# Optimization experiments

Hardware: AMD Instinct MI355X
Metric: run time of the kernel (lower is better)

The kernel has to match this reference:

```python
import jax, jax.numpy as jnp
import numpy as np

LOC_SIZE, LOC_EMB = 100000, 256
TIM_SIZE, TIM_EMB = 48, 64
UID_SIZE, UID_EMB = 5000, 128
HID = 512
B, T = 64, 128
L_HIST, G = 1024, 4  # 256 history groups of size 4


def setup_inputs() -> dict:
    key = jax.random.key(0)
    ks = jax.random.split(key, 16)
    s = 0.02
    inp = {
        "loc": jax.random.randint(ks[0], (B, T), 0, LOC_SIZE),
        "tim": jax.random.randint(ks[1], (B, T), 0, TIM_SIZE),
        "input_lengths": jax.random.randint(ks[2], (B,), 1, T + 1),
        "history_loc": jax.random.randint(ks[3], (B, L_HIST), 0, LOC_SIZE),
        "history_tim": jax.random.randint(ks[4], (B, L_HIST), 0, TIM_SIZE),
        "history_uid": jax.random.randint(ks[5], (B, L_HIST), 0, UID_SIZE),
        "group_size": G,
        "emb_loc": jax.random.normal(ks[6], (LOC_SIZE, LOC_EMB), jnp.float32) * s,
        "emb_tim": jax.random.normal(ks[7], (TIM_SIZE, TIM_EMB), jnp.float32) * s,
        "emb_uid": jax.random.normal(ks[8], (UID_SIZE, UID_EMB), jnp.float32) * s,
        "W_attn": jax.random.normal(ks[9], (HID, LOC_EMB + TIM_EMB + UID_EMB), jnp.float32) * s,
        "b_attn": jnp.zeros((HID,), jnp.float32),
        "W_ih": jax.random.normal(ks[10], (3 * HID, LOC_EMB + TIM_EMB), jnp.float32) * s,
        "b_ih": jnp.zeros((3 * HID,), jnp.float32),
        "W_hh": jax.random.normal(ks[11], (3 * HID, HID), jnp.float32) * s,
        "b_hh": jnp.zeros((3 * HID,), jnp.float32),
        "W_final": jax.random.normal(ks[12], (UID_SIZE, 3 * HID), jnp.float32) * s,
        "b_final": jnp.zeros((UID_SIZE,), jnp.float32),
    }
    return inp


def _gru(x_seq, W_ih, b_ih, W_hh, b_hh):
    # x_seq: [T, B, Din] -> outputs [T, B, H], PyTorch gate order (r, z, n)
    H = W_hh.shape[1]
    gx = jnp.einsum("tbd,gd->tbg", x_seq, W_ih) + b_ih  # [T,B,3H]
    h0 = jnp.zeros((x_seq.shape[1], H), x_seq.dtype)

    def step(h, gx_t):
        gh = h @ W_hh.T + b_hh
        xr, xz, xn = jnp.split(gx_t, 3, axis=-1)
        hr, hz, hn = jnp.split(gh, 3, axis=-1)
        r = jax.nn.sigmoid(xr + hr)
        z = jax.nn.sigmoid(xz + hz)
        n = jnp.tanh(xn + r * hn)
        h_new = (1.0 - z) * n + z * h
        return h_new, h_new

    _, outs = jax.lax.scan(step, h0, gx)
    return outs  # [T,B,H]


def reference(loc, tim, input_lengths, history_loc, history_tim, history_uid,
              group_size, emb_loc, emb_tim, emb_uid, W_attn, b_attn,
              W_ih, b_ih, W_hh, b_hh, W_final, b_final):
    Bn, Tn = loc.shape
    # current-trajectory embeddings -> GRU (dropout is identity in eval)
    x = jnp.concatenate([emb_loc[loc], emb_tim[tim]], axis=-1)  # [B,T,Din]
    outs = _gru(jnp.swapaxes(x, 0, 1), W_ih, b_ih, W_hh, b_hh)  # [T,B,H]
    outs = jnp.swapaxes(outs, 0, 1)                              # [B,T,H]
    last = outs[jnp.arange(Bn), input_lengths - 1]               # [B,H]

    # history pooling: groups of size G; uid emb averaged within group,
    # loc/tim embeddings taken at each group's first element
    Gc = group_size
    n_groups = history_uid.shape[1] // Gc
    uid_h = emb_uid[history_uid].reshape(Bn, n_groups, Gc, -1).mean(axis=2)  # [B,N,Du]
    loc_h = emb_loc[history_loc[:, ::Gc]]                                    # [B,N,Dl]
    tim_h = emb_tim[history_tim[:, ::Gc]]                                    # [B,N,Dt]
    hist = jnp.concatenate([loc_h, tim_h, uid_h], axis=-1)
    hist = jnp.tanh(jnp.einsum("bnd,hd->bnh", hist, W_attn) + b_attn)        # [B,N,H]

    # 'dot' attention: replaces the nested python-loop scoring
    energies = jnp.einsum("bh,bnh->bn", last, hist)
    attn_w = jax.nn.softmax(energies, axis=-1)
    context = jnp.einsum("bn,bnh->bh", attn_w, hist)

    out = jnp.concatenate([last, context, last], axis=-1)  # [B,3H]
    y = out @ W_final.T + b_final                          # [B,U]
    # original assigns y (one row) into score[t] of shape [T,U] -> broadcast over T
    score = jnp.broadcast_to(y[:, None, :], (Bn, Tn, y.shape[-1]))
    return score
```

## Files before the change

kernel.cpp:

```cpp
#include <hip/hip_runtime.h>
#include <hip/hip_bf16.h>


typedef __attribute__((ext_vector_type(8))) short bf16x8;
typedef __attribute__((ext_vector_type(4))) float f32x4;
typedef __attribute__((ext_vector_type(4))) unsigned short u16x4;
typedef __attribute__((ext_vector_type(2))) unsigned long long u64x2;
typedef unsigned long long u64;

__device__ inline unsigned short f2bf(float x) {
  __hip_bfloat16 b = __float2bfloat16(x);
  return __builtin_bit_cast(unsigned short, b);
}
__device__ inline bf16x8 pack8(float4 a, float4 b) {
  bf16x8 w;
  w[0]=(short)f2bf(a.x); w[1]=(short)f2bf(a.y); w[2]=(short)f2bf(a.z); w[3]=(short)f2bf(a.w);
  w[4]=(short)f2bf(b.x); w[5]=(short)f2bf(b.y); w[6]=(short)f2bf(b.z); w[7]=(short)f2bf(b.w);
  return w;
}

__global__ __launch_bounds__(256)
void gemm_gx_f(const int* __restrict__ loc, const int* __restrict__ tim,
               const float* __restrict__ eloc, const float* __restrict__ etim,
               const float* __restrict__ W_ih, const float* __restrict__ b_ih,
               float* __restrict__ gx) {
  constexpr int LDR = 40, K = 320, N = 1536;
  __shared__ short Asl[128 * LDR];
  __shared__ short Bsl[128 * LDR];
  const int tid = threadIdx.x;
  const int lane = tid & 63, wid = tid >> 6;
  const int wr = wid >> 1, wc = wid & 1;
  const int m16 = lane & 15, g4 = lane >> 4;
  const int bm = blockIdx.y * 128, bn = blockIdx.x * 128;
  const int srow = tid >> 1, shalf = tid & 1;
  f32x4 acc[4][4] = {};
  for (int k0 = 0; k0 < K; k0 += 32) {
    {
      const int grow = bm + srow;
      const int t = grow >> 6, b = grow & 63;
      const float* ap = (k0 < 256)
        ? eloc + (size_t)loc[b * 128 + t] * 256 + k0 + (shalf << 4)
        : etim + (size_t)tim[b * 128 + t] * 64 + (k0 - 256) + (shalf << 4);
      float4 f0 = ((const float4*)ap)[0], f1 = ((const float4*)ap)[1];
      float4 f2 = ((const float4*)ap)[2], f3 = ((const float4*)ap)[3];
      short* arow = Asl + srow * LDR + (shalf << 4);
      *(bf16x8*)(arow)     = pack8(f0, f1);
      *(bf16x8*)(arow + 8) = pack8(f2, f3);
      const float* bp = W_ih + (size_t)(bn + srow) * K + k0 + (shalf << 4);
      f0 = ((const float4*)bp)[0]; f1 = ((const float4*)bp)[1];
      f2 = ((const float4*)bp)[2]; f3 = ((const float4*)bp)[3];
      short* brow = Bsl + srow * LDR + (shalf << 4);
      *(bf16x8*)(brow)     = pack8(f0, f1);
      *(bf16x8*)(brow + 8) = pack8(f2, f3);
    }
    __syncthreads();
    bf16x8 af[4], bfr[4];
#pragma unroll
    for (int i = 0; i < 4; ++i) {
      af[i]  = *(const bf16x8*)(Asl + ((wr << 6) + (i << 4) + m16) * LDR + (g4 << 3));
      bfr[i] = *(const bf16x8*)(Bsl + ((wc << 6) + (i << 4) + m16) * LDR + (g4 << 3));
    }
#pragma unroll
    for (int i = 0; i < 4; ++i)
#pragma unroll
      for (int j = 0; j < 4; ++j)
        acc[i][j] = __builtin_amdgcn_mfma_f32_16x16x32_bf16(af[i], bfr[j], acc[i][j], 0, 0, 0);
    __syncthreads();
  }
#pragma unroll
  for (int i = 0; i < 4; ++i)
#pragma unroll
    for (int j = 0; j < 4; ++j) {
      const int col = bn + (wc << 6) + (j << 4) + m16;
      const float bv = b_ih[col];
#pragma unroll
      for (int q = 0; q < 4; ++q) {
        const int row = bm + (wr << 6) + (i << 4) + (g4 << 2) + q;
        gx[(size_t)row * N + col] = acc[i][j][q] + bv;
      }
    }
}

__global__ __launch_bounds__(256)
void gemm_attn_f(const int* __restrict__ hloc, const int* __restrict__ htim,
                 const int* __restrict__ huid,
                 const float* __restrict__ eloc, const float* __restrict__ etim,
                 const float* __restrict__ euid,
                 const float* __restrict__ W_attn, const float* __restrict__ b_attn,
                 float* __restrict__ histt) {
  constexpr int LDR = 40, K = 448, N = 512;
  __shared__ short Asl[128 * LDR];
  __shared__ short Bsl[128 * LDR];
  const int tid = threadIdx.x;
  const int lane = tid & 63, wid = tid >> 6;
  const int wr = wid >> 1, wc = wid & 1;
  const int m16 = lane & 15, g4 = lane >> 4;
  const int bm = blockIdx.y * 128, bn = blockIdx.x * 128;
  const int srow = tid >> 1, shalf = tid & 1;
  f32x4 acc[4][4] = {};
  for (int k0 = 0; k0 < K; k0 += 32) {
    {
      const int grow = bm + srow;
      const int b = grow >> 8, n = grow & 255;
      const int base = b * 1024 + (n << 2);
      float4 f0, f1, f2, f3;
      if (k0 < 256) {
        const float* ap = eloc + (size_t)hloc[base] * 256 + k0 + (shalf << 4);
        f0 = ((const float4*)ap)[0]; f1 = ((const float4*)ap)[1];
        f2 = ((const float4*)ap)[2]; f3 = ((const float4*)ap)[3];
      } else if (k0 < 320) {
        const float* ap = etim + (size_t)htim[base] * 64 + (k0 - 256) + (shalf << 4);
        f0 = ((const float4*)ap)[0]; f1 = ((const float4*)ap)[1];
        f2 = ((const float4*)ap)[2]; f3 = ((const float4*)ap)[3];
      } else {
        const int cu = (k0 - 320) + (shalf << 4);
        const float4* u0 = (const float4*)(euid + (size_t)huid[base + 0] * 128 + cu);
        const float4* u1 = (const float4*)(euid + (size_t)huid[base + 1] * 128 + cu);
        const float4* u2 = (const float4*)(euid + (size_t)huid[base + 2] * 128 + cu);
        const float4* u3 = (const float4*)(euid + (size_t)huid[base + 3] * 128 + cu);
#define AVG4(idx, dst) { float4 a=u0[idx],b4=u1[idx],c4=u2[idx],d4=u3[idx];            \
        dst.x=0.25f*(a.x+b4.x+c4.x+d4.x); dst.y=0.25f*(a.y+b4.y+c4.y+d4.y);           \
        dst.z=0.25f*(a.z+b4.z+c4.z+d4.z); dst.w=0.25f*(a.w+b4.w+c4.w+d4.w); }
        AVG4(0, f0) AVG4(1, f1) AVG4(2, f2) AVG4(3, f3)
#undef AVG4
      }
      short* arow = Asl + srow * LDR + (shalf << 4);
      *(bf16x8*)(arow)     = pack8(f0, f1);
      *(bf16x8*)(arow + 8) = pack8(f2, f3);
      const float* bp = W_attn + (size_t)(bn + srow) * K + k0 + (shalf << 4);
      f0 = ((const float4*)bp)[0]; f1 = ((const float4*)bp)[1];
      f2 = ((const float4*)bp)[2]; f3 = ((const float4*)bp)[3];
      short* brow = Bsl + srow * LDR + (shalf << 4);
      *(bf16x8*)(brow)     = pack8(f0, f1);
      *(bf16x8*)(brow + 8) = pack8(f2, f3);
    }
    __syncthreads();
    bf16x8 af[4], bfr[4];
#pragma unroll
    for (int i = 0; i < 4; ++i) {
      af[i]  = *(const bf16x8*)(Asl + ((wr << 6) + (i << 4) + m16) * LDR + (g4 << 3));
      bfr[i] = *(const bf16x8*)(Bsl + ((wc << 6) + (i << 4) + m16) * LDR + (g4 << 3));
    }
#pragma unroll
    for (int i = 0; i < 4; ++i)
#pragma unroll
      for (int j = 0; j < 4; ++j)
        acc[i][j] = __builtin_amdgcn_mfma_f32_16x16x32_bf16(af[i], bfr[j], acc[i][j], 0, 0, 0);
    __syncthreads();
  }
#pragma unroll
  for (int i = 0; i < 4; ++i)
#pragma unroll
    for (int j = 0; j < 4; ++j) {
      const int col = bn + (wc << 6) + (j << 4) + m16;
      const float bv = b_attn[col];
#pragma unroll
      for (int q = 0; q < 4; ++q) {
        const int row = bm + (wr << 6) + (i << 4) + (g4 << 2) + q;
        histt[(size_t)row * N + col] = tanhf(acc[i][j][q] + bv);
      }
    }
}

__global__ __launch_bounds__(128)
void gru_persist(const float* __restrict__ gx, const float* __restrict__ W_hh,
                 const float* __restrict__ b_hh, const int* __restrict__ lens,
                 short* __restrict__ h_bf, float* __restrict__ lastb,
                 unsigned int* __restrict__ flags) {
  __shared__ short wlds[6 * 16 * 512];
  const int tid = threadIdx.x;
  const int lane = tid & 63, tt = tid >> 6;
  const int bid = blockIdx.x;
  const int c = bid >> 2, grp = bid & 3;
  const int j0 = (c << 5) + (tt << 4);
  const int b0 = grp << 4;
  const int m16 = lane & 15, g4 = lane >> 4;

  for (int gi = 0; gi < 3; ++gi) {
    const float* wg = W_hh + (size_t)(gi * 512 + j0) * 512;
    short* slab = wlds + (((gi << 1) + tt) << 13);
    for (int r = 0; r < 16; ++r) {
      int k = lane << 3;
      const float4* src = (const float4*)(wg + (size_t)r * 512 + k);
      int off = ((r << 9) + k) ^ ((r & 7) << 3);
      *(bf16x8*)(slab + off) = pack8(src[0], src[1]);
    }
  }
  __syncthreads();

  const int bcol = b0 + m16;
  const int jr = j0 + (g4 << 2);
  const f32x4 bhr = *(const f32x4*)&b_hh[jr];
  const f32x4 bhz = *(const f32x4*)&b_hh[512 + jr];
  const f32x4 bhn = *(const f32x4*)&b_hh[1024 + jr];
  const int lenb = lens[bcol];
  f32x4 hprev = {0.f, 0.f, 0.f, 0.f};

  unsigned int* gflags = flags + (grp << 8);
  unsigned int* ownflag = gflags + (c << 4);

  for (int t = 0; t < 128; ++t) {
    const float* gxb = gx + ((size_t)t * 64 + bcol) * 1536;
    f32x4 gr = *(const f32x4*)(gxb + jr);
    f32x4 gz = *(const f32x4*)(gxb + 512 + jr);
    f32x4 gn = *(const f32x4*)(gxb + 1024 + jr);
    f32x4 ar = {0.f, 0.f, 0.f, 0.f}, az = ar, an = ar;
    if (t) {
      unsigned tgt = (unsigned)t;
      while (true) {
        unsigned f = tgt;
        if (lane < 16)
          f = __hip_atomic_load(gflags + (lane << 4), __ATOMIC_RELAXED, __HIP_MEMORY_SCOPE_AGENT);
        if (__all((int)(f >= tgt))) break;
      }
      asm volatile("" ::: "memory");

      const u64* hp = (const u64*)(h_bf + ((t & 1) << 15) + (size_t)bcol * 512 + (g4 << 3));
      u64 hu[32];
#pragma unroll
      for (int ks = 0; ks < 16; ++ks) {
        hu[2 * ks]     = __hip_atomic_load(hp + ks * 8,     __ATOMIC_RELAXED, __HIP_MEMORY_SCOPE_AGENT);
        hu[2 * ks + 1] = __hip_atomic_load(hp + ks * 8 + 1, __ATOMIC_RELAXED, __HIP_MEMORY_SCOPE_AGENT);
      }
#define GRU_MFMA(ks)                                                                 \
      {                                                                              \
        u64x2 p; p[0] = hu[2 * (ks)]; p[1] = hu[2 * (ks) + 1];                       \
        bf16x8 hf = __builtin_bit_cast(bf16x8, p);                                   \
        int off = ((m16 << 9) + ((ks) << 5) + (g4 << 3)) ^ ((m16 & 7) << 3);         \
        ar = __builtin_amdgcn_mfma_f32_16x16x32_bf16(*(const bf16x8*)(wlds + ((0 + tt) << 13) + off), hf, ar, 0, 0, 0); \
        az = __builtin_amdgcn_mfma_f32_16x16x32_bf16(*(const bf16x8*)(wlds + ((2 + tt) << 13) + off), hf, az, 0, 0, 0); \
        an = __builtin_amdgcn_mfma_f32_16x16x32_bf16(*(const bf16x8*)(wlds + ((4 + tt) << 13) + off), hf, an, 0, 0, 0); \
      }
      GRU_MFMA(0)  GRU_MFMA(1)  GRU_MFMA(2)  GRU_MFMA(3)
      GRU_MFMA(4)  GRU_MFMA(5)  GRU_MFMA(6)  GRU_MFMA(7)
      GRU_MFMA(8)  GRU_MFMA(9)  GRU_MFMA(10) GRU_MFMA(11)
      GRU_MFMA(12) GRU_MFMA(13) GRU_MFMA(14) GRU_MFMA(15)
#undef GRU_MFMA
    }
    u16x4 hw;
#pragma unroll
    for (int q = 0; q < 4; ++q) {
      float r = 1.f / (1.f + __expf(-(gr[q] + ar[q] + bhr[q])));
      float z = 1.f / (1.f + __expf(-(gz[q] + az[q] + bhz[q])));
      float xn = gn[q] + r * (an[q] + bhn[q]);
      float n = 1.f - 2.f / (__expf(2.f * xn) + 1.f);
      float hv = (1.f - z) * n + z * hprev[q];
      hprev[q] = hv;
      hw[q] = f2bf(hv);
    }
    __hip_atomic_store((u64*)(h_bf + ((~t & 1) << 15) + (size_t)bcol * 512 + jr),
                       __builtin_bit_cast(u64, hw),
                       __ATOMIC_RELAXED, __HIP_MEMORY_SCOPE_AGENT);
    if (t == lenb - 1) {
      *(f32x4*)(lastb + (size_t)bcol * 512 + jr) = hprev;
    }
    if (t < 127) {
      asm volatile("s_waitcnt vmcnt(0)" ::: "memory");
      __syncthreads();
      if (tid == 0)
        __hip_atomic_store(ownflag, (unsigned)(t + 1), __ATOMIC_RELAXED, __HIP_MEMORY_SCOPE_AGENT);
    }
  }
}

__global__ __launch_bounds__(256)
void attn_ctx(const float* __restrict__ histt, const float* __restrict__ last,
              float* __restrict__ ctx) {
  int b = blockIdx.x, tid = threadIdx.x;
  __shared__ float ls[512];
  __shared__ float w[256];
  __shared__ float red[256];
  ((float2*)ls)[tid] = ((const float2*)(last + (size_t)b * 512))[tid];
  __syncthreads();
  const float* hb = histt + (size_t)b * 256 * 512;
  const float* hrow = hb + (size_t)tid * 512;
  float acc = 0.f;
  for (int k = 0; k < 512; k += 4) {
    float4 h4 = *(const float4*)(hrow + k);
    acc += ls[k] * h4.x + ls[k + 1] * h4.y + ls[k + 2] * h4.z + ls[k + 3] * h4.w;
  }
  red[tid] = acc;
  __syncthreads();
  for (int s = 128; s; s >>= 1) {
    if (tid < s) red[tid] = fmaxf(red[tid], red[tid + s]);
    __syncthreads();
  }
  float m = red[0];
  __syncthreads();
  float ex = expf(acc - m);
  w[tid] = ex; red[tid] = ex;
  __syncthreads();
  for (int s = 128; s; s >>= 1) {
    if (tid < s) red[tid] += red[tid + s];
    __syncthreads();
  }
  float inv = 1.f / red[0];
  float c0 = 0.f, c1 = 0.f;
  for (int n = 0; n < 256; ++n) {
    float wn = w[n];
    c0 += wn * hb[(size_t)n * 512 + tid];
    c1 += wn * hb[(size_t)n * 512 + tid + 256];
  }
  ctx[(size_t)b * 512 + tid]       = c0 * inv;
  ctx[(size_t)b * 512 + tid + 256] = c1 * inv;
}

__global__ __launch_bounds__(256)
void final_gemm(const float* __restrict__ last, const float* __restrict__ ctx,
                const float* __restrict__ Wf, const float* __restrict__ bf,
                float* __restrict__ y) {
  __shared__ float s[64][132];
  const int tid = threadIdx.x;
  const int u0 = blockIdx.x << 3;
  const int ul = tid >> 6, b = tid & 63;
  float acc0 = 0.f, acc1 = 0.f;
  for (int kc = 0; kc < 12; ++kc) {
    __syncthreads();
    for (int i = tid; i < 2048; i += 256) {
      int rb = i >> 5, cc = (i & 31) << 2;
      int k = kc * 128 + cc;
      const float* src = (k < 512) ? (last + (size_t)rb * 512 + k)
                       : (k < 1024) ? (ctx + (size_t)rb * 512 + k - 512)
                                    : (last + (size_t)rb * 512 + k - 1024);
      *(float4*)&s[rb][cc] = *(const float4*)src;
    }
    __syncthreads();
#pragma unroll
    for (int uu = 0; uu < 2; ++uu) {
      int u = u0 + ul + uu * 4;
      const float* wrow = Wf + (size_t)u * 1536 + kc * 128;
      float a = 0.f;
#pragma unroll 8
      for (int c = 0; c < 128; c += 4) {
        float4 w4 = *(const float4*)(wrow + c);
        float4 s4 = *(const float4*)&s[b][c];
        a += w4.x * s4.x + w4.y * s4.y + w4.z * s4.z + w4.w * s4.w;
      }
      if (uu == 0) acc0 += a; else acc1 += a;
    }
  }
  int u = u0 + ul;
  y[(size_t)b * 5000 + u]     = acc0 + bf[u];
  y[(size_t)b * 5000 + u + 4] = acc1 + bf[u + 4];
}

__global__ void broadcast_y(const float* __restrict__ y, float* __restrict__ out) {
  int bt = blockIdx.x;
  const float4* src = (const float4*)(y + (size_t)(bt >> 7) * 5000);
  float4* dst = (float4*)(out + (size_t)bt * 5000);
  for (int i = threadIdx.x; i < 1250; i += 256) dst[i] = src[i];
}

extern "C" void kernel_launch(void* const* d_in, const int* in_sizes, int n_in,
                              void* d_out, int out_size, void* d_ws, size_t ws_size,
                              hipStream_t stream) {
  const int* loc  = (const int*)d_in[0];
  const int* tim  = (const int*)d_in[1];
  const int* lens = (const int*)d_in[2];
  const int* hloc = (const int*)d_in[3];
  const int* htim = (const int*)d_in[4];
  const int* huid = (const int*)d_in[5];
  const float* eloc    = (const float*)d_in[7];
  const float* etim    = (const float*)d_in[8];
  const float* euid    = (const float*)d_in[9];
  const float* W_attn  = (const float*)d_in[10];
  const float* b_attn  = (const float*)d_in[11];
  const float* W_ih    = (const float*)d_in[12];
  const float* b_ih    = (const float*)d_in[13];
  const float* W_hh    = (const float*)d_in[14];
  const float* b_hh    = (const float*)d_in[15];
  const float* W_final = (const float*)d_in[16];
  const float* b_final = (const float*)d_in[17];
  float* out = (float*)d_out;
  char* ws = (char*)d_ws;

  float* gx    = (float*)(ws + 0ull);
  float* histt = (float*)(ws + 50331648ull);
  float* lastb = (float*)(ws + 83886080ull);
  float* ctx   = (float*)(ws + 84017152ull);
  float* yv    = (float*)(ws + 84148224ull);
  short* h_bf  = (short*)(ws + 85428224ull);
  unsigned int* flags = (unsigned int*)(ws + 85559296ull);

  gemm_gx_f<<<dim3(12, 64), 256, 0, stream>>>(loc, tim, eloc, etim, W_ih, b_ih, gx);
  gemm_attn_f<<<dim3(4, 128), 256, 0, stream>>>(hloc, htim, huid, eloc, etim, euid,
                                                W_attn, b_attn, histt);

  hipMemsetAsync(flags, 0, 4096, stream);
  gru_persist<<<64, 128, 0, stream>>>(gx, W_hh, b_hh, lens, h_bf, lastb, flags);

  attn_ctx<<<64, 256, 0, stream>>>(histt, lastb, ctx);
  final_gemm<<<625, 256, 0, stream>>>(lastb, ctx, W_final, b_final, yv);
  broadcast_y<<<8192, 256, 0, stream>>>(yv, out);
}
```

Before: 685.6 us.

## Fuse GRU recurrence and history attention GEMM into one heterogeneous kernel

Merges the persistent GRU kernel and the history-projection GEMM into a single launch of 192 blocks. The first 64 blocks run the latency-bound GRU recurrence and the other 128 blocks loop over the 512 attention GEMM tiles at the same time. This hides the attention GEMM behind the serial GRU and removes one launch. In exchange, GRU blocks now use 256 threads, half of which only sit at barriers, and the GEMM blocks may contend with the GRU for memory bandwidth and CU resources.

```diff
diff --git a/kernel.cpp b/kernel.cpp
--- a/kernel.cpp
+++ b/kernel.cpp
@@ -82,184 +82,192 @@
 }
 
 __global__ __launch_bounds__(256)
-void gemm_attn_f(const int* __restrict__ hloc, const int* __restrict__ htim,
-                 const int* __restrict__ huid,
-                 const float* __restrict__ eloc, const float* __restrict__ etim,
-                 const float* __restrict__ euid,
-                 const float* __restrict__ W_attn, const float* __restrict__ b_attn,
-                 float* __restrict__ histt) {
+void gru_attn(const float* __restrict__ gx, const float* __restrict__ W_hh,
+              const float* __restrict__ b_hh, const int* __restrict__ lens,
+              short* __restrict__ h_bf, float* __restrict__ lastb,
+              unsigned int* __restrict__ flags,
+              const int* __restrict__ hloc, const int* __restrict__ htim,
+              const int* __restrict__ huid,
+              const float* __restrict__ eloc, const float* __restrict__ etim,
+              const float* __restrict__ euid,
+              const float* __restrict__ W_attn, const float* __restrict__ b_attn,
+              float* __restrict__ histt) {
+  __shared__ short smem[6 * 16 * 512];
+  const int bid = blockIdx.x;
+  const int tid = threadIdx.x;
+
+  if (bid < 64) {
+    if (tid >= 128) {
+      for (int t = 0; t < 128; ++t) __syncthreads();
+      return;
+    }
+    const int lane = tid & 63, tt = tid >> 6;
+    const int c = bid >> 2, grp = bid & 3;
+    const int j0 = (c << 5) + (tt << 4);
+    const int b0 = grp << 4;
+    const int m16 = lane & 15, g4 = lane >> 4;
+
+    for (int gi = 0; gi < 3; ++gi) {
+      const float* wg = W_hh + (size_t)(gi * 512 + j0) * 512;
+      short* slab = smem + (((gi << 1) + tt) << 13);
+      for (int r = 0; r < 16; ++r) {
+        int k = lane << 3;
+        const float4* src = (const float4*)(wg + (size_t)r * 512 + k);
+        int off = ((r << 9) + k) ^ ((r & 7) << 3);
+        *(bf16x8*)(slab + off) = pack8(src[0], src[1]);
+      }
+    }
+    __syncthreads();
+
+    const int bcol = b0 + m16;
+    const int jr = j0 + (g4 << 2);
+    const f32x4 bhr = *(const f32x4*)&b_hh[jr];
+    const f32x4 bhz = *(const f32x4*)&b_hh[512 + jr];
+    const f32x4 bhn = *(const f32x4*)&b_hh[1024 + jr];
+    const int lenb = lens[bcol];
+    f32x4 hprev = {0.f, 0.f, 0.f, 0.f};
+
+    unsigned int* gflags = flags + (grp << 8);
+    unsigned int* ownflag = gflags + (c << 4);
+
+    for (int t = 0; t < 128; ++t) {
+      const float* gxb = gx + ((size_t)t * 64 + bcol) * 1536;
+      f32x4 gr = *(const f32x4*)(gxb + jr);
+      f32x4 gz = *(const f32x4*)(gxb + 512 + jr);
+      f32x4 gn = *(const f32x4*)(gxb + 1024 + jr);
+      f32x4 ar = {0.f, 0.f, 0.f, 0.f}, az = ar, an = ar;
+      if (t) {
+        unsigned tgt = (unsigned)t;
+        while (true) {
+          unsigned f = tgt;
+          if (lane < 16)
+            f = __hip_atomic_load(gflags + (lane << 4), __ATOMIC_RELAXED, __HIP_MEMORY_SCOPE_AGENT);
+          if (__all((int)(f >= tgt))) break;
+        }
+        asm volatile("" ::: "memory");
+
+        const u64* hp = (const u64*)(h_bf + ((t & 1) << 15) + (size_t)bcol * 512 + (g4 << 3));
+        u64 hu[32];
+#pragma unroll
+        for (int ks = 0; ks < 16; ++ks) {
+          hu[2 * ks]     = __hip_atomic_load(hp + ks * 8,     __ATOMIC_RELAXED, __HIP_MEMORY_SCOPE_AGENT);
+          hu[2 * ks + 1] = __hip_atomic_load(hp + ks * 8 + 1, __ATOMIC_RELAXED, __HIP_MEMORY_SCOPE_AGENT);
+        }
+#define GRU_MFMA(ks)                                                                 \
+        {                                                                            \
+          u64x2 p; p[0] = hu[2 * (ks)]; p[1] = hu[2 * (ks) + 1];                     \
+          bf16x8 hf = __builtin_bit_cast(bf16x8, p);                                 \
+          int off = ((m16 << 9) + ((ks) << 5) + (g4 << 3)) ^ ((m16 & 7) << 3);       \
+          ar = __builtin_amdgcn_mfma_f32_16x16x32_bf16(*(const bf16x8*)(smem + ((0 + tt) << 13) + off), hf, ar, 0, 0, 0); \
+          az = __builtin_amdgcn_mfma_f32_16x16x32_bf16(*(const bf16x8*)(smem + ((2 + tt) << 13) + off), hf, az, 0, 0, 0); \
+          an = __builtin_amdgcn_mfma_f32_16x16x32_bf16(*(const bf16x8*)(smem + ((4 + tt) << 13) + off), hf, an, 0, 0, 0); \
+        }
+        GRU_MFMA(0)  GRU_MFMA(1)  GRU_MFMA(2)  GRU_MFMA(3)
+        GRU_MFMA(4)  GRU_MFMA(5)  GRU_MFMA(6)  GRU_MFMA(7)
+        GRU_MFMA(8)  GRU_MFMA(9)  GRU_MFMA(10) GRU_MFMA(11)
+        GRU_MFMA(12) GRU_MFMA(13) GRU_MFMA(14) GRU_MFMA(15)
+#undef GRU_MFMA
+      }
+      u16x4 hw;
+#pragma unroll
+      for (int q = 0; q < 4; ++q) {
+        float r = 1.f / (1.f + __expf(-(gr[q] + ar[q] + bhr[q])));
+        float z = 1.f / (1.f + __expf(-(gz[q] + az[q] + bhz[q])));
+        float xn = gn[q] + r * (an[q] + bhn[q]);
+        float n = 1.f - 2.f / (__expf(2.f * xn) + 1.f);
+        float hv = (1.f - z) * n + z * hprev[q];
+        hprev[q] = hv;
+        hw[q] = f2bf(hv);
+      }
+      __hip_atomic_store((u64*)(h_bf + ((~t & 1) << 15) + (size_t)bcol * 512 + jr),
+                         __builtin_bit_cast(u64, hw),
+                         __ATOMIC_RELAXED, __HIP_MEMORY_SCOPE_AGENT);
+      if (t == lenb - 1) {
+        *(f32x4*)(lastb + (size_t)bcol * 512 + jr) = hprev;
+      }
+      if (t < 127) {
+        asm volatile("s_waitcnt vmcnt(0)" ::: "memory");
+        __syncthreads();
+        if (tid == 0)
+          __hip_atomic_store(ownflag, (unsigned)(t + 1), __ATOMIC_RELAXED, __HIP_MEMORY_SCOPE_AGENT);
+      }
+    }
+    return;
+  }
+
   constexpr int LDR = 40, K = 448, N = 512;
-  __shared__ short Asl[128 * LDR];
-  __shared__ short Bsl[128 * LDR];
-  const int tid = threadIdx.x;
+  short* Asl = smem;
+  short* Bsl = smem + 128 * LDR;
   const int lane = tid & 63, wid = tid >> 6;
   const int wr = wid >> 1, wc = wid & 1;
   const int m16 = lane & 15, g4 = lane >> 4;
-  const int bm = blockIdx.y * 128, bn = blockIdx.x * 128;
   const int srow = tid >> 1, shalf = tid & 1;
-  f32x4 acc[4][4] = {};
-  for (int k0 = 0; k0 < K; k0 += 32) {
-    {
-      const int grow = bm + srow;
-      const int b = grow >> 8, n = grow & 255;
-      const int base = b * 1024 + (n << 2);
-      float4 f0, f1, f2, f3;
-      if (k0 < 256) {
-        const float* ap = eloc + (size_t)hloc[base] * 256 + k0 + (shalf << 4);
-        f0 = ((const float4*)ap)[0]; f1 = ((const float4*)ap)[1];
-        f2 = ((const float4*)ap)[2]; f3 = ((const float4*)ap)[3];
-      } else if (k0 < 320) {
-        const float* ap = etim + (size_t)htim[base] * 64 + (k0 - 256) + (shalf << 4);
-        f0 = ((const float4*)ap)[0]; f1 = ((const float4*)ap)[1];
-        f2 = ((const float4*)ap)[2]; f3 = ((const float4*)ap)[3];
-      } else {
-        const int cu = (k0 - 320) + (shalf << 4);
-        const float4* u0 = (const float4*)(euid + (size_t)huid[base + 0] * 128 + cu);
-        const float4* u1 = (const float4*)(euid + (size_t)huid[base + 1] * 128 + cu);
-        const float4* u2 = (const float4*)(euid + (size_t)huid[base + 2] * 128 + cu);
-        const float4* u3 = (const float4*)(euid + (size_t)huid[base + 3] * 128 + cu);
+  for (int tile = bid - 64; tile < 512; tile += 128) {
+    const int yt = tile >> 2, nt = tile & 3;
+    const int bm = yt << 7, bn = nt << 7;
+    f32x4 acc[4][4] = {};
+    for (int k0 = 0; k0 < K; k0 += 32) {
+      {
+        const int grow = bm + srow;
+        const int b = grow >> 8, n = grow & 255;
+        const int base = b * 1024 + (n << 2);
+        float4 f0, f1, f2, f3;
+        if (k0 < 256) {
+          const float* ap = eloc + (size_t)hloc[base] * 256 + k0 + (shalf << 4);
+          f0 = ((const float4*)ap)[0]; f1 = ((const float4*)ap)[1];
+          f2 = ((const float4*)ap)[2]; f3 = ((const float4*)ap)[3];
+        } else if (k0 < 320) {
+          const float* ap = etim + (size_t)htim[base] * 64 + (k0 - 256) + (shalf << 4);
+          f0 = ((const float4*)ap)[0]; f1 = ((const float4*)ap)[1];
+          f2 = ((const float4*)ap)[2]; f3 = ((const float4*)ap)[3];
+        } else {
+          const int cu = (k0 - 320) + (shalf << 4);
+          const float4* u0 = (const float4*)(euid + (size_t)huid[base + 0] * 128 + cu);
+          const float4* u1 = (const float4*)(euid + (size_t)huid[base + 1] * 128 + cu);
+          const float4* u2 = (const float4*)(euid + (size_t)huid[base + 2] * 128 + cu);
+          const float4* u3 = (const float4*)(euid + (size_t)huid[base + 3] * 128 + cu);
 #define AVG4(idx, dst) { float4 a=u0[idx],b4=u1[idx],c4=u2[idx],d4=u3[idx];            \
-        dst.x=0.25f*(a.x+b4.x+c4.x+d4.x); dst.y=0.25f*(a.y+b4.y+c4.y+d4.y);           \
-        dst.z=0.25f*(a.z+b4.z+c4.z+d4.z); dst.w=0.25f*(a.w+b4.w+c4.w+d4.w); }
-        AVG4(0, f0) AVG4(1, f1) AVG4(2, f2) AVG4(3, f3)
+          dst.x=0.25f*(a.x+b4.x+c4.x+d4.x); dst.y=0.25f*(a.y+b4.y+c4.y+d4.y);         \
+          dst.z=0.25f*(a.z+b4.z+c4.z+d4.z); dst.w=0.25f*(a.w+b4.w+c4.w+d4.w); }
+          AVG4(0, f0) AVG4(1, f1) AVG4(2, f2) AVG4(3, f3)
 #undef AVG4
-      }
-      short* arow = Asl + srow * LDR + (shalf << 4);
-      *(bf16x8*)(arow)     = pack8(f0, f1);
-      *(bf16x8*)(arow + 8) = pack8(f2, f3);
-      const float* bp = W_attn + (size_t)(bn + srow) * K + k0 + (shalf << 4);
-      f0 = ((const float4*)bp)[0]; f1 = ((const float4*)bp)[1];
-      f2 = ((const float4*)bp)[2]; f3 = ((const float4*)bp)[3];
-      short* brow = Bsl + srow * LDR + (shalf << 4);
-      *(bf16x8*)(brow)     = pack8(f0, f1);
-      *(bf16x8*)(brow + 8) = pack8(f2, f3);
-    }
-    __syncthreads();
-    bf16x8 af[4], bfr[4];
-#pragma unroll
-    for (int i = 0; i < 4; ++i) {
-      af[i]  = *(const bf16x8*)(Asl + ((wr << 6) + (i << 4) + m16) * LDR + (g4 << 3));
-      bfr[i] = *(const bf16x8*)(Bsl + ((wc << 6) + (i << 4) + m16) * LDR + (g4 << 3));
+        }
+        short* arow = Asl + srow * LDR + (shalf << 4);
+        *(bf16x8*)(arow)     = pack8(f0, f1);
+        *(bf16x8*)(arow + 8) = pack8(f2, f3);
+        const float* bp = W_attn + (size_t)(bn + srow) * K + k0 + (shalf << 4);
+        f0 = ((const float4*)bp)[0]; f1 = ((const float4*)bp)[1];
+        f2 = ((const float4*)bp)[2]; f3 = ((const float4*)bp)[3];
+        short* brow = Bsl + srow * LDR + (shalf << 4);
+        *(bf16x8*)(brow)     = pack8(f0, f1);
+        *(bf16x8*)(brow + 8) = pack8(f2, f3);
+      }
+      __syncthreads();
+      bf16x8 af[4], bfr[4];
+#pragma unroll
+      for (int i = 0; i < 4; ++i) {
+        af[i]  = *(const bf16x8*)(Asl + ((wr << 6) + (i << 4) + m16) * LDR + (g4 << 3));
+        bfr[i] = *(const bf16x8*)(Bsl + ((wc << 6) + (i << 4) + m16) * LDR + (g4 << 3));
+      }
+#pragma unroll
+      for (int i = 0; i < 4; ++i)
+#pragma unroll
+        for (int j = 0; j < 4; ++j)
+          acc[i][j] = __builtin_amdgcn_mfma_f32_16x16x32_bf16(af[i], bfr[j], acc[i][j], 0, 0, 0);
+      __syncthreads();
     }
 #pragma unroll
     for (int i = 0; i < 4; ++i)
 #pragma unroll
-      for (int j = 0; j < 4; ++j)
-        acc[i][j] = __builtin_amdgcn_mfma_f32_16x16x32_bf16(af[i], bfr[j], acc[i][j], 0, 0, 0);
-    __syncthreads();
-  }
-#pragma unroll
-  for (int i = 0; i < 4; ++i)
-#pragma unroll
-    for (int j = 0; j < 4; ++j) {
-      const int col = bn + (wc << 6) + (j << 4) + m16;
-      const float bv = b_attn[col];
-#pragma unroll
-      for (int q = 0; q < 4; ++q) {
-        const int row = bm + (wr << 6) + (i << 4) + (g4 << 2) + q;
-        histt[(size_t)row * N + col] = tanhf(acc[i][j][q] + bv);
-      }
-    }
-}
-
-__global__ __launch_bounds__(128)
-void gru_persist(const float* __restrict__ gx, const float* __restrict__ W_hh,
-                 const float* __restrict__ b_hh, const int* __restrict__ lens,
-                 short* __restrict__ h_bf, float* __restrict__ lastb,
-                 unsigned int* __restrict__ flags) {
-  __shared__ short wlds[6 * 16 * 512];
-  const int tid = threadIdx.x;
-  const int lane = tid & 63, tt = tid >> 6;
-  const int bid = blockIdx.x;
-  const int c = bid >> 2, grp = bid & 3;
-  const int j0 = (c << 5) + (tt << 4);
-  const int b0 = grp << 4;
-  const int m16 = lane & 15, g4 = lane >> 4;
-
-  for (int gi = 0; gi < 3; ++gi) {
-    const float* wg = W_hh + (size_t)(gi * 512 + j0) * 512;
-    short* slab = wlds + (((gi << 1) + tt) << 13);
-    for (int r = 0; r < 16; ++r) {
-      int k = lane << 3;
-      const float4* src = (const float4*)(wg + (size_t)r * 512 + k);
-      int off = ((r << 9) + k) ^ ((r & 7) << 3);
-      *(bf16x8*)(slab + off) = pack8(src[0], src[1]);
-    }
-  }
-  __syncthreads();
-
-  const int bcol = b0 + m16;
-  const int jr = j0 + (g4 << 2);
-  const f32x4 bhr = *(const f32x4*)&b_hh[jr];
-  const f32x4 bhz = *(const f32x4*)&b_hh[512 + jr];
-  const f32x4 bhn = *(const f32x4*)&b_hh[1024 + jr];
-  const int lenb = lens[bcol];
-  f32x4 hprev = {0.f, 0.f, 0.f, 0.f};
-
-  unsigned int* gflags = flags + (grp << 8);
-  unsigned int* ownflag = gflags + (c << 4);
-
-  for (int t = 0; t < 128; ++t) {
-    const float* gxb = gx + ((size_t)t * 64 + bcol) * 1536;
-    f32x4 gr = *(const f32x4*)(gxb + jr);
-    f32x4 gz = *(const f32x4*)(gxb + 512 + jr);
-    f32x4 gn = *(const f32x4*)(gxb + 1024 + jr);
-    f32x4 ar = {0.f, 0.f, 0.f, 0.f}, az = ar, an = ar;
-    if (t) {
-      unsigned tgt = (unsigned)t;
-      while (true) {
-        unsigned f = tgt;
-        if (lane < 16)
-          f = __hip_atomic_load(gflags + (lane << 4), __ATOMIC_RELAXED, __HIP_MEMORY_SCOPE_AGENT);
-        if (__all((int)(f >= tgt))) break;
-      }
-      asm volatile("" ::: "memory");
-
-      const u64* hp = (const u64*)(h_bf + ((t & 1) << 15) + (size_t)bcol * 512 + (g4 << 3));
-      u64 hu[32];
-#pragma unroll
-      for (int ks = 0; ks < 16; ++ks) {
-        hu[2 * ks]     = __hip_atomic_load(hp + ks * 8,     __ATOMIC_RELAXED, __HIP_MEMORY_SCOPE_AGENT);
-        hu[2 * ks + 1] = __hip_atomic_load(hp + ks * 8 + 1, __ATOMIC_RELAXED, __HIP_MEMORY_SCOPE_AGENT);
-      }
-#define GRU_MFMA(ks)                                                                 \
-      {                                                                              \
-        u64x2 p; p[0] = hu[2 * (ks)]; p[1] = hu[2 * (ks) + 1];                       \
-        bf16x8 hf = __builtin_bit_cast(bf16x8, p);                                   \
-        int off = ((m16 << 9) + ((ks) << 5) + (g4 << 3)) ^ ((m16 & 7) << 3);         \
-        ar = __builtin_amdgcn_mfma_f32_16x16x32_bf16(*(const bf16x8*)(wlds + ((0 + tt) << 13) + off), hf, ar, 0, 0, 0); \
-        az = __builtin_amdgcn_mfma_f32_16x16x32_bf16(*(const bf16x8*)(wlds + ((2 + tt) << 13) + off), hf, az, 0, 0, 0); \
-        an = __builtin_amdgcn_mfma_f32_16x16x32_bf16(*(const bf16x8*)(wlds + ((4 + tt) << 13) + off), hf, an, 0, 0, 0); \
-      }
-      GRU_MFMA(0)  GRU_MFMA(1)  GRU_MFMA(2)  GRU_MFMA(3)
-      GRU_MFMA(4)  GRU_MFMA(5)  GRU_MFMA(6)  GRU_MFMA(7)
-      GRU_MFMA(8)  GRU_MFMA(9)  GRU_MFMA(10) GRU_MFMA(11)
-      GRU_MFMA(12) GRU_MFMA(13) GRU_MFMA(14) GRU_MFMA(15)
-#undef GRU_MFMA
-    }
-    u16x4 hw;
-#pragma unroll
-    for (int q = 0; q < 4; ++q) {
-      float r = 1.f / (1.f + __expf(-(gr[q] + ar[q] + bhr[q])));
-      float z = 1.f / (1.f + __expf(-(gz[q] + az[q] + bhz[q])));
-      float xn = gn[q] + r * (an[q] + bhn[q]);
-      float n = 1.f - 2.f / (__expf(2.f * xn) + 1.f);
-      float hv = (1.f - z) * n + z * hprev[q];
-      hprev[q] = hv;
-      hw[q] = f2bf(hv);
-    }
-    __hip_atomic_store((u64*)(h_bf + ((~t & 1) << 15) + (size_t)bcol * 512 + jr),
-                       __builtin_bit_cast(u64, hw),
-                       __ATOMIC_RELAXED, __HIP_MEMORY_SCOPE_AGENT);
-    if (t == lenb - 1) {
-      *(f32x4*)(lastb + (size_t)bcol * 512 + jr) = hprev;
-    }
-    if (t < 127) {
-      asm volatile("s_waitcnt vmcnt(0)" ::: "memory");
-      __syncthreads();
-      if (tid == 0)
-        __hip_atomic_store(ownflag, (unsigned)(t + 1), __ATOMIC_RELAXED, __HIP_MEMORY_SCOPE_AGENT);
-    }
+      for (int j = 0; j < 4; ++j) {
+        const int col = bn + (wc << 6) + (j << 4) + m16;
+        const float bv = b_attn[col];
+#pragma unroll
+        for (int q = 0; q < 4; ++q) {
+          const int row = bm + (wr << 6) + (i << 4) + (g4 << 2) + q;
+          histt[(size_t)row * N + col] = tanhf(acc[i][j][q] + bv);
+        }
+      }
   }
 }
 
@@ -382,12 +390,12 @@
   short* h_bf  = (short*)(ws + 85428224ull);
   unsigned int* flags = (unsigned int*)(ws + 85559296ull);
 
+  hipMemsetAsync(flags, 0, 4096, stream);
   gemm_gx_f<<<dim3(12, 64), 256, 0, stream>>>(loc, tim, eloc, etim, W_ih, b_ih, gx);
-  gemm_attn_f<<<dim3(4, 128), 256, 0, stream>>>(hloc, htim, huid, eloc, etim, euid,
-                                                W_attn, b_attn, histt);
-
-  hipMemsetAsync(flags, 0, 4096, stream);
-  gru_persist<<<64, 128, 0, stream>>>(gx, W_hh, b_hh, lens, h_bf, lastb, flags);
+
+  gru_attn<<<192, 256, 0, stream>>>(gx, W_hh, b_hh, lens, h_bf, lastb, flags,
+                                    hloc, htim, huid, eloc, etim, euid,
+                                    W_attn, b_attn, histt);
 
   attn_ctx<<<64, 256, 0, stream>>>(histt, lastb, ctx);
   final_gemm<<<625, 256, 0, stream>>>(lastb, ctx, W_final, b_final, yv);
```

Measured after the change: 645.6 us. -5.8%, faster.
